# Optimization experiments

Hardware: AMD Instinct MI355X
Metric: run time of the kernel (lower is better)

Reference implementation:

```python
import jax, jax.numpy as jnp
import numpy as np

N_RAYS = 131072
N_SAMPLES = 64
N_IMP = 64
BBALL_RADIUS = 1.0


def sample_pdf_det(bins, weights, n_samples):
    # bins: [N, S], weights: [N, S-1]; deterministic inverse-CDF sampling (det=True)
    weights = weights + 1e-5
    pdf = weights / jnp.sum(weights, -1, keepdims=True)
    cdf = jnp.cumsum(pdf, -1)
    cdf = jnp.concatenate([jnp.zeros_like(cdf[..., :1]), cdf], -1)  # [N, S]
    u = jnp.linspace(0.5 / n_samples, 1.0 - 0.5 / n_samples, n_samples, dtype=cdf.dtype)
    u = jnp.broadcast_to(u, cdf.shape[:-1] + (n_samples,))
    inds = jax.vmap(lambda c, uu: jnp.searchsorted(c, uu, side='right'))(cdf, u)
    below = jnp.maximum(inds - 1, 0)
    above = jnp.minimum(inds, cdf.shape[-1] - 1)
    cdf_b = jnp.take_along_axis(cdf, below, -1)
    cdf_a = jnp.take_along_axis(cdf, above, -1)
    bins_b = jnp.take_along_axis(bins, below, -1)
    bins_a = jnp.take_along_axis(bins, above, -1)
    denom = cdf_a - cdf_b
    denom = jnp.where(denom < 1e-5, jnp.ones_like(denom), denom)
    t = (u - cdf_b) / denom
    return bins_b + t * (bins_a - bins_b)


def setup_inputs() -> dict:
    key = jax.random.key(0)
    k1, k2, k3, k4 = jax.random.split(key, 4)
    rays_o = jax.random.normal(k1, (N_RAYS, 3), jnp.float32) * 0.1
    d = jax.random.normal(k2, (N_RAYS, 3), jnp.float32)
    rays_d = d / jnp.linalg.norm(d, axis=-1, keepdims=True)
    near = 0.5 + 0.1 * jax.random.uniform(k3, (N_RAYS, 1), jnp.float32)
    far = near + 1.5
    t = jnp.linspace(0.0, 1.0, N_SAMPLES, dtype=jnp.float32)
    z_vals = near + (far - near) * t[None, :]  # sorted along samples, per NeuS render_normal
    sdf = jax.random.normal(k4, (N_RAYS, N_SAMPLES), jnp.float32)
    return {"rays_o": rays_o, "rays_d": rays_d, "z_vals": z_vals, "sdf": sdf,
            "n_importance": N_IMP, "inv_s": 64}


def reference(rays_o, rays_d, z_vals, sdf, n_importance, inv_s):
    # NeuSRenderer.up_sample: SDF -> alpha -> cumprod weights -> inverse-CDF resample
    inv_s = jnp.float32(inv_s)
    pts = rays_o[:, None, :] + rays_d[:, None, :] * z_vals[..., :, None]  # [N, S, 3]
    radius = jnp.linalg.norm(pts, axis=-1)  # [N, S]
    inside_sphere = ((radius[:, :-1] < BBALL_RADIUS) | (radius[:, 1:] < BBALL_RADIUS)).astype(z_vals.dtype)
    prev_sdf, next_sdf = sdf[:, :-1], sdf[:, 1:]
    prev_z, next_z = z_vals[:, :-1], z_vals[:, 1:]
    mid_sdf = (prev_sdf + next_sdf) * 0.5
    cos_val = (next_sdf - prev_sdf) / (next_z - prev_z + 1e-5)
    prev_cos_val = jnp.concatenate([jnp.zeros_like(cos_val[:, :1]), cos_val[:, :-1]], -1)
    cos_val = jnp.minimum(prev_cos_val, cos_val)
    cos_val = jnp.clip(cos_val, -1e3, 0.0) * inside_sphere
    dist = next_z - prev_z
    prev_esti_sdf = mid_sdf - cos_val * dist * 0.5
    next_esti_sdf = mid_sdf + cos_val * dist * 0.5
    prev_cdf = jax.nn.sigmoid(prev_esti_sdf * inv_s)
    next_cdf = jax.nn.sigmoid(next_esti_sdf * inv_s)
    alpha = (prev_cdf - next_cdf + 1e-5) / (prev_cdf + 1e-5)  # [N, S-1]
    trans = jnp.cumprod(jnp.concatenate([jnp.ones_like(alpha[:, :1]), 1.0 - alpha + 1e-7], -1), -1)[:, :-1]
    weights = alpha * trans  # [N, S-1]
    z_samples = sample_pdf_det(z_vals, weights, n_importance)  # [N, n_importance]
    return z_samples
```

## Files before the change

kernel.cpp:

```cpp
#include <hip/hip_runtime.h>


template<int CTRL, int RM>
__device__ __forceinline__ float dpp_movf(float old, float x) {
    return __int_as_float(__builtin_amdgcn_update_dpp(
        __float_as_int(old), __float_as_int(x), CTRL, RM, 0xF, false));
}
__device__ __forceinline__ float fast_rcp(float x) { return __builtin_amdgcn_rcpf(x); }
__device__ __forceinline__ float bperm(float x, int srclane) {
    return __int_as_float(__builtin_amdgcn_ds_bpermute(srclane << 2, __float_as_int(x)));
}

__global__ __launch_bounds__(256) void neus_upsample_kernel(
    const float* __restrict__ rays_o,
    const float* __restrict__ rays_d,
    const float* __restrict__ z_vals,
    const float* __restrict__ sdf,
    const int*   __restrict__ inv_s_ptr,
    float*       __restrict__ out,
    int n_rays)
{
    __shared__ float cdf_s[16][68];

    const int tid  = threadIdx.x;
    const int lane = tid & 63;
    const int L    = lane & 15;
    const int slot = tid >> 4;
    const int ray  = blockIdx.x * 16 + slot;
    if (ray >= n_rays) return;

    const float inv_s = (float)inv_s_ptr[0];

    const float4 zc = *(const float4*)(z_vals + ray * 64 + 4 * L);
    const float4 sc = *(const float4*)(sdf    + ray * 64 + 4 * L);
    const float ox = rays_o[ray*3+0], oy = rays_o[ray*3+1], oz = rays_o[ray*3+2];
    const float dx = rays_d[ray*3+0], dy = rays_d[ray*3+1], dz_ = rays_d[ray*3+2];
    const float a  = ox*ox + oy*oy + oz*oz;
    const float b2 = 2.0f * (ox*dx + oy*dy + oz*dz_);

    const float z4 = dpp_movf<0x130, 0xF>(zc.x, zc.x);
    const float s4 = dpp_movf<0x130, 0xF>(sc.x, sc.x);

    const float zv[5] = {zc.x, zc.y, zc.z, zc.w, z4};
    const float sv[5] = {sc.x, sc.y, sc.z, sc.w, s4};

    float r2[5];
    #pragma unroll
    for (int e = 0; e < 5; ++e) r2[e] = fmaf(zv[e], zv[e] + b2, a);

    float cr[4];
    #pragma unroll
    for (int e = 0; e < 4; ++e)
        cr[e] = (sv[e+1] - sv[e]) * fast_rcp(zv[e+1] - zv[e] + 1e-5f);

    float prev = dpp_movf<0x111, 0xF>(0.0f, cr[3]);

    float alpha[4], pp[4];
    float prun = 1.0f;
    #pragma unroll
    for (int e = 0; e < 4; ++e) {
        float cosv = fminf(prev, cr[e]); prev = cr[e];
        cosv = fminf(fmaxf(cosv, -1000.0f), 0.0f);
        cosv = (fminf(r2[e], r2[e+1]) < 1.0f) ? cosv : 0.0f;
        const float mid = 0.5f * (sv[e] + sv[e+1]);
        const float hd  = 0.5f * (zv[e+1] - zv[e]);
        const float pe  = fmaf(-cosv, hd, mid);
        const float ne  = fmaf( cosv, hd, mid);
        const float pcf = fast_rcp(1.0f + __expf(-pe * inv_s));
        const float ncf = fast_rcp(1.0f + __expf(-ne * inv_s));
        alpha[e] = (pcf - ncf + 1e-5f) * fast_rcp(pcf + 1e-5f);
        pp[e] = prun;
        prun *= (1.0f - alpha[e] + 1e-7f);
    }

    float IP = prun;
    IP *= dpp_movf<0x111, 0xF>(1.0f, IP);
    IP *= dpp_movf<0x112, 0xF>(1.0f, IP);
    IP *= dpp_movf<0x114, 0xF>(1.0f, IP);
    IP *= dpp_movf<0x118, 0xF>(1.0f, IP);
    const float Pex = dpp_movf<0x111, 0xF>(1.0f, IP);

    float cl[4];
    float ssum = 0.0f;
    #pragma unroll
    for (int e = 0; e < 4; ++e) {
        float we = fmaf(alpha[e] * pp[e], Pex, 1e-5f);
        if (e == 3) we = (L == 15) ? 0.0f : we;
        cl[e] = ssum;
        ssum += we;
    }

    float IS = ssum;
    IS += dpp_movf<0x111, 0xF>(0.0f, IS);
    IS += dpp_movf<0x112, 0xF>(0.0f, IS);
    IS += dpp_movf<0x114, 0xF>(0.0f, IS);
    IS += dpp_movf<0x118, 0xF>(0.0f, IS);
    const float Sex = dpp_movf<0x111, 0xF>(0.0f, IS);

    const float T    = bperm(IS, lane | 15);
    const float rtot = fast_rcp(T);
    const float Ert  = Sex * rtot;
    const float z0   = bperm(zc.x, lane & 48);
    const float z63  = bperm(zc.w, lane | 15);
    const float h    = (z63 - z0) * (1.0f / 63.0f);

    float4 cvec;
    cvec.x = fmaf(cl[0], rtot, Ert);
    cvec.y = fmaf(cl[1], rtot, Ert);
    cvec.z = fmaf(cl[2], rtot, Ert);
    cvec.w = fmaf(cl[3], rtot, Ert);
    *(float4*)(&cdf_s[slot][4 * L]) = cvec;

    const float* cp = cdf_s[slot];
    const float kbase = (float)(4 * L);
    float ov[4];
    #pragma unroll
    for (int e = 0; e < 4; ++e) {
        const float u = fmaf(kbase + (float)e, 0.015625f, 0.0078125f);
        int pos = 0;
        #pragma unroll
        for (int st = 32; st; st >>= 1) {
            const float c = cp[pos + st - 1];
            if (c <= u) pos += st;
        }
        const float cb = cp[pos - 1];
        const float ca = cp[pos];
        float gap = ca - cb;
        gap = (gap < 1e-5f) ? 1.0f : gap;
        const float t = (u - cb) * fast_rcp(gap);
        ov[e] = fmaf((float)(pos - 1) + t, h, z0);
    }
    *(float4*)(out + ray * 64 + 4 * L) = make_float4(ov[0], ov[1], ov[2], ov[3]);
}

extern "C" void kernel_launch(void* const* d_in, const int* in_sizes, int n_in,
                              void* d_out, int out_size, void* d_ws, size_t ws_size,
                              hipStream_t stream) {
    const float* rays_o = (const float*)d_in[0];
    const float* rays_d = (const float*)d_in[1];
    const float* z_vals = (const float*)d_in[2];
    const float* sdf    = (const float*)d_in[3];
    const int*   inv_s  = (const int*)d_in[5];
    float* out = (float*)d_out;

    const int n_rays = in_sizes[0] / 3;
    const int blocks = (n_rays + 15) / 16;

    neus_upsample_kernel<<<blocks, 256, 0, stream>>>(
        rays_o, rays_d, z_vals, sdf, inv_s, out, n_rays);
}
```

Baseline: 117.0 us.

## Replace per-sample binary search with scatter-max bucket marking and prefix max

Drops the 6-step LDS binary search per output sample. Each CDF entry instead computes the first uniform sample index it covers and atomically marks it in shared memory. A running max across lanes (DPP prefix max) then gives each sample its bracketing bin directly. This trades the dependent LDS loads for LDS atomics and an extra scan, and relies on the u values being uniform and the CDF being monotone. Exact matching of the right-side searchsorted at floating-point boundaries is a risk.

Result: no change. 115.0 us (-1.6%).

```diff
diff --git a/kernel.cpp b/kernel.cpp
--- a/kernel.cpp
+++ b/kernel.cpp
@@ -5,6 +5,10 @@
 __device__ __forceinline__ float dpp_movf(float old, float x) {
     return __int_as_float(__builtin_amdgcn_update_dpp(
         __float_as_int(old), __float_as_int(x), CTRL, RM, 0xF, false));
+}
+template<int CTRL, int RM>
+__device__ __forceinline__ int dpp_movi(int old, int x) {
+    return __builtin_amdgcn_update_dpp(old, x, CTRL, RM, 0xF, false);
 }
 __device__ __forceinline__ float fast_rcp(float x) { return __builtin_amdgcn_rcpf(x); }
 __device__ __forceinline__ float bperm(float x, int srclane) {
@@ -21,6 +25,7 @@
     int n_rays)
 {
     __shared__ float cdf_s[16][68];
+    __shared__ int   mark_s[16][64];
 
     const int tid  = threadIdx.x;
     const int lane = tid & 63;
@@ -110,25 +115,46 @@
     cvec.z = fmaf(cl[2], rtot, Ert);
     cvec.w = fmaf(cl[3], rtot, Ert);
     *(float4*)(&cdf_s[slot][4 * L]) = cvec;
+    *(int4*)(&mark_s[slot][4 * L]) = make_int4(0, 0, 0, 0);
+    __builtin_amdgcn_wave_barrier();
+
+    const float Cv[4] = {cvec.x, cvec.y, cvec.z, cvec.w};
+    #pragma unroll
+    for (int e = 0; e < 4; ++e) {
+        const int kj = (int)ceilf(fmaf(64.0f, Cv[e], -0.5f));
+        if (kj < 64) atomicMax(&mark_s[slot][kj], 4 * L + e);
+    }
+    __builtin_amdgcn_wave_barrier();
+
+    const int4 m4 = *(const int4*)(&mark_s[slot][4 * L]);
+    const int i0 = m4.x;
+    const int i1 = max(i0, m4.y);
+    const int i2 = max(i1, m4.z);
+    const int i3 = max(i2, m4.w);
+
+    int ms = i3;
+    ms = max(ms, dpp_movi<0x111, 0xF>(0, ms));
+    ms = max(ms, dpp_movi<0x112, 0xF>(0, ms));
+    ms = max(ms, dpp_movi<0x114, 0xF>(0, ms));
+    ms = max(ms, dpp_movi<0x118, 0xF>(0, ms));
+    const int Mex = dpp_movi<0x111, 0xF>(0, ms);
+
+    const int bl[4] = { min(max(Mex, i0), 62), min(max(Mex, i1), 62),
+                        min(max(Mex, i2), 62), min(max(Mex, i3), 62) };
 
     const float* cp = cdf_s[slot];
     const float kbase = (float)(4 * L);
     float ov[4];
     #pragma unroll
     for (int e = 0; e < 4; ++e) {
-        const float u = fmaf(kbase + (float)e, 0.015625f, 0.0078125f);
-        int pos = 0;
-        #pragma unroll
-        for (int st = 32; st; st >>= 1) {
-            const float c = cp[pos + st - 1];
-            if (c <= u) pos += st;
-        }
-        const float cb = cp[pos - 1];
-        const float ca = cp[pos];
+        const float u  = fmaf(kbase + (float)e, 0.015625f, 0.0078125f);
+        const int   b  = bl[e];
+        const float cb = cp[b];
+        const float ca = cp[b + 1];
         float gap = ca - cb;
         gap = (gap < 1e-5f) ? 1.0f : gap;
         const float t = (u - cb) * fast_rcp(gap);
-        ov[e] = fmaf((float)(pos - 1) + t, h, z0);
+        ov[e] = fmaf((float)b + t, h, z0);
     }
     *(float4*)(out + ray * 64 + 4 * L) = make_float4(ov[0], ov[1], ov[2], ov[3]);
 }
```
